# Optimization experiments

Hardware: AMD Instinct MI355X
Metric: run time of the kernel (lower is better)

## Reference

```python
import jax, jax.numpy as jnp
import numpy as np

N, E, G = 50000, 500000, 8
IN, HID, OUT, NC, H = 256, 128, 64, 10, 2
NPG = N // G  # nodes per graph
NEG_SLOPE = 0.2


def setup_inputs() -> dict:
    key = jax.random.key(0)
    ks = jax.random.split(key, 24)
    x = jax.random.normal(ks[0], (N, IN), jnp.float32)
    # edges constrained to stay within each graph, no self-loops
    src = jax.random.randint(ks[1], (E,), 0, N)
    base = (src // NPG) * NPG
    off = jax.random.randint(ks[2], (E,), 1, NPG)
    dst = base + (src - base + off) % NPG
    edge_index = jnp.stack([src, dst], axis=0).astype(jnp.int32)
    edge_attr = jax.random.uniform(ks[3], (E, 1), jnp.float32)
    batch = jnp.repeat(jnp.arange(G, dtype=jnp.int32), NPG)
    y = jax.random.randint(ks[4], (N,), 0, NC).astype(jnp.int32)

    s = 0.1
    p = {
        'W1': jax.random.normal(ks[5], (IN, H * HID), jnp.float32) * s,
        'att_src1': jax.random.normal(ks[6], (H, HID), jnp.float32) * s,
        'att_dst1': jax.random.normal(ks[7], (H, HID), jnp.float32) * s,
        'We1': jax.random.normal(ks[8], (1, H * HID), jnp.float32) * s,
        'att_edge1': jax.random.normal(ks[9], (H, HID), jnp.float32) * s,
        'b1': jnp.zeros((HID,), jnp.float32),
        'W2': jax.random.normal(ks[10], (HID, H * OUT), jnp.float32) * s,
        'att_src2': jax.random.normal(ks[11], (H, OUT), jnp.float32) * s,
        'att_dst2': jax.random.normal(ks[12], (H, OUT), jnp.float32) * s,
        'We2': jax.random.normal(ks[13], (1, H * OUT), jnp.float32) * s,
        'att_edge2': jax.random.normal(ks[14], (H, OUT), jnp.float32) * s,
        'b2': jnp.zeros((OUT,), jnp.float32),
        'Wc': jax.random.normal(ks[15], (OUT, NC), jnp.float32) * s,
        'bc': jnp.zeros((NC,), jnp.float32),
    }
    return dict(x=x, edge_index=edge_index, edge_attr=edge_attr, batch=batch, y=y, **p)


def _gat_layer(x, src, dst, eattr, W, a_src, a_dst, We, a_e, b, n_nodes, C):
    # PyG GATConv: heads=H, concat=False (mean over heads), edge_dim features.
    xp = (x @ W).reshape(n_nodes, H, C)                    # [N,H,C]
    al_s = jnp.einsum('nhc,hc->nh', xp, a_src)             # [N,H]
    al_d = jnp.einsum('nhc,hc->nh', xp, a_dst)
    ef = (eattr @ We).reshape(-1, H, C)                    # [E,H,C]
    al_e = jnp.einsum('ehc,hc->eh', ef, a_e)               # [E,H]
    alpha = jax.nn.leaky_relu(al_s[src] + al_d[dst] + al_e, NEG_SLOPE)
    # edge softmax grouped by destination (every dst has a self-loop -> no empty segs)
    m = jax.ops.segment_max(alpha, dst, num_segments=n_nodes)
    ex = jnp.exp(alpha - m[dst])
    denom = jax.ops.segment_sum(ex, dst, num_segments=n_nodes)
    w = ex / (denom[dst] + 1e-16)                          # [E,H]
    msg = xp[src] * w[:, :, None]                          # [E,H,C]
    out = jax.ops.segment_sum(msg, dst, num_segments=n_nodes)  # [N,H,C]
    return out.mean(axis=1) + b


def reference(x, edge_index, edge_attr, batch, y,
              W1, att_src1, att_dst1, We1, att_edge1, b1,
              W2, att_src2, att_dst2, We2, att_edge2, b2,
              Wc, bc):
    src, dst = edge_index[0], edge_index[1]
    # add self-loops; edge_attr fill = per-graph mean (as in the per-graph loop)
    g = batch[src]
    cnt = jax.ops.segment_sum(jnp.ones_like(edge_attr[:, 0]), g, num_segments=G)
    mean_attr = jax.ops.segment_sum(edge_attr, g, num_segments=G) / cnt[:, None]
    loop_attr = mean_attr[batch]                           # [N,1]
    ar = jnp.arange(N, dtype=src.dtype)
    src_a = jnp.concatenate([src, ar])
    dst_a = jnp.concatenate([dst, ar])
    ea = jnp.concatenate([edge_attr, loop_attr], axis=0)

    h = _gat_layer(x, src_a, dst_a, ea, W1, att_src1, att_dst1, We1, att_edge1, b1, N, HID)
    h = jax.nn.relu(h)
    h = _gat_layer(h, src_a, dst_a, ea, W2, att_src2, att_dst2, We2, att_edge2, b2, N, OUT)
    pred = h @ Wc + bc                                     # [N,NC]
    return pred, y
```

## Files before the change

### kernel.cpp

```cpp
#include <hip/hip_runtime.h>
#include <hip/hip_bf16.h>
#include <cstdint>
#include <cstddef>

#define N_NODES 50000
#define N_EDGES 500000
#define EA_EDGES 550000
#define NPG 6250
#define G_GRAPHS 8
#define IN_DIM 256
#define HID_DIM 128
#define OUT_DIM 64
#define NCLS 10
#define NEG_SLOPE 0.2f

typedef __attribute__((ext_vector_type(8))) short short8v;
typedef __attribute__((ext_vector_type(4))) float f32x4;

__device__ __forceinline__ unsigned short f2bf(float f) {
  __hip_bfloat16 h = __float2bfloat16(f);
  unsigned short u;
  __builtin_memcpy(&u, &h, 2);
  return u;
}
__device__ __forceinline__ float bf2f(unsigned short u) {
  return __uint_as_float(((unsigned)u) << 16);
}

__global__ void k_sums_degree(const int* __restrict__ src, const int* __restrict__ dst,
                              const float* __restrict__ eattr,
                              float* __restrict__ sums, float* __restrict__ cnts,
                              int* __restrict__ deg) {
  __shared__ float ls[G_GRAPHS], lc[G_GRAPHS];
  if (threadIdx.x < G_GRAPHS) { ls[threadIdx.x] = 0.f; lc[threadIdx.x] = 0.f; }
  __syncthreads();
  int stride = gridDim.x * blockDim.x;
  for (int e = blockIdx.x * blockDim.x + threadIdx.x; e < EA_EDGES; e += stride) {
    if (e < N_EDGES) {
      int g = src[e] / NPG;
      atomicAdd(&ls[g], eattr[e]);
      atomicAdd(&lc[g], 1.f);
      atomicAdd(&deg[dst[e]], 1);
    } else {
      atomicAdd(&deg[e - N_EDGES], 1);
    }
  }
  __syncthreads();
  if (threadIdx.x < G_GRAPHS) {
    atomicAdd(&sums[threadIdx.x], ls[threadIdx.x]);
    atomicAdd(&cnts[threadIdx.x], lc[threadIdx.x]);
  }
}

__global__ void k_prep(const float* __restrict__ sums, const float* __restrict__ cnts,
                       float* __restrict__ mean,
                       const float* __restrict__ We1, const float* __restrict__ ae1,
                       const float* __restrict__ We2, const float* __restrict__ ae2,
                       float* __restrict__ ce) {
  if (threadIdx.x == 0 && blockIdx.x == 0) {
    for (int g = 0; g < G_GRAPHS; ++g) mean[g] = sums[g] / cnts[g];
    for (int h = 0; h < 2; ++h) {
      float s = 0.f;
      for (int c = 0; c < HID_DIM; ++c) s += We1[h * HID_DIM + c] * ae1[h * HID_DIM + c];
      ce[h] = s;
    }
    for (int h = 0; h < 2; ++h) {
      float s = 0.f;
      for (int c = 0; c < OUT_DIM; ++c) s += We2[h * OUT_DIM + c] * ae2[h * OUT_DIM + c];
      ce[2 + h] = s;
    }
  }
}

__global__ void k_scan1(const int* __restrict__ deg, int* __restrict__ rowptr,
                        int* __restrict__ bsum, int n) {
  __shared__ int sm[1024];
  int tid = threadIdx.x;
  int i = blockIdx.x * 1024 + tid;
  int v = (i < n) ? deg[i] : 0;
  sm[tid] = v;
  __syncthreads();
  for (int off = 1; off < 1024; off <<= 1) {
    int t = (tid >= off) ? sm[tid - off] : 0;
    __syncthreads();
    if (tid >= off) sm[tid] += t;
    __syncthreads();
  }
  if (i < n) rowptr[i] = sm[tid] - v;
  if (tid == 1023) bsum[blockIdx.x] = sm[1023];
}

__global__ void k_scan2(int* __restrict__ bsum, int* __restrict__ rowptr, int nb, int n) {
  if (threadIdx.x == 0 && blockIdx.x == 0) {
    int run = 0;
    for (int i = 0; i < nb; ++i) { int v = bsum[i]; bsum[i] = run; run += v; }
    rowptr[n] = run;
  }
}

__global__ void k_scan3(int* __restrict__ rowptr, int* __restrict__ cursor,
                        const int* __restrict__ bsum, int n) {
  int i = blockIdx.x * blockDim.x + threadIdx.x;
  if (i < n) {
    int r = rowptr[i] + bsum[i >> 10];
    rowptr[i] = r;
    cursor[i] = r;
  }
}

__global__ void k_fill(const int* __restrict__ src, const int* __restrict__ dst,
                       const float* __restrict__ eattr, const float* __restrict__ mean,
                       int* __restrict__ cursor, int2* __restrict__ csr) {
  int e = blockIdx.x * blockDim.x + threadIdx.x;
  if (e >= EA_EDGES) return;
  int s, d; float a;
  if (e < N_EDGES) { s = src[e]; d = dst[e]; a = eattr[e]; }
  else { int i = e - N_EDGES; s = i; d = i; a = mean[i / NPG]; }
  int p = atomicAdd(&cursor[d], 1);
  csr[p] = make_int2(s, __float_as_int(a));
}

__global__ void k_cast_bf16(const float* __restrict__ in, unsigned short* __restrict__ out, int n8) {
  int i = blockIdx.x * blockDim.x + threadIdx.x;
  if (i >= n8) return;
  float4 a = *(const float4*)(in + (size_t)i * 8);
  float4 b = *(const float4*)(in + (size_t)i * 8 + 4);
  uint4 o;
  o.x = (unsigned)f2bf(a.x) | ((unsigned)f2bf(a.y) << 16);
  o.y = (unsigned)f2bf(a.z) | ((unsigned)f2bf(a.w) << 16);
  o.z = (unsigned)f2bf(b.x) | ((unsigned)f2bf(b.y) << 16);
  o.w = (unsigned)f2bf(b.z) | ((unsigned)f2bf(b.w) << 16);
  *(uint4*)(out + (size_t)i * 8) = o;
}

__global__ void k_cast_t(const float* __restrict__ W, unsigned short* __restrict__ Wt,
                         int K, int N) {
  int i = blockIdx.x * blockDim.x + threadIdx.x;
  if (i >= K * N) return;
  int k = i / N, n = i - k * N;
  Wt[(size_t)n * K + k] = f2bf(W[i]);
}

template <int K>
__global__ __launch_bounds__(256) void k_gemm_mfma(const unsigned short* __restrict__ A,
                                                   const unsigned short* __restrict__ Bt,
                                                   unsigned short* __restrict__ C,
                                                   int M, int Nout) {
  constexpr int BM = 128, BN = 128, BK = 64;
  __shared__ __attribute__((aligned(16))) unsigned short As[BM * BK];
  __shared__ __attribute__((aligned(16))) unsigned short Bs[BN * BK];
  const int tid = threadIdx.x;
  const int lane = tid & 63;
  const int wid = tid >> 6;
  const int wr = wid >> 1, wc = wid & 1;
  const int r0 = blockIdx.y * BM, c0 = blockIdx.x * BN;
  f32x4 acc[4][4] = {};

  for (int k0 = 0; k0 < K; k0 += BK) {
#pragma unroll
    for (int i = 0; i < 4; ++i) {
      int c = tid + i * 256;
      int row = c >> 3, kc = c & 7;
      int gr = r0 + row;
      uint4 v = make_uint4(0, 0, 0, 0);
      if (gr < M) v = *(const uint4*)(A + (size_t)gr * K + k0 + kc * 8);
      int boff = (row * 128 + kc * 16) ^ ((row & 7) << 4);
      *(uint4*)((char*)As + boff) = v;
    }
#pragma unroll
    for (int i = 0; i < 4; ++i) {
      int c = tid + i * 256;
      int row = c >> 3, kc = c & 7;
      uint4 v = *(const uint4*)(Bt + (size_t)(c0 + row) * K + k0 + kc * 8);
      int boff = (row * 128 + kc * 16) ^ ((row & 7) << 4);
      *(uint4*)((char*)Bs + boff) = v;
    }
    __syncthreads();
#pragma unroll
    for (int ks = 0; ks < 2; ++ks) {
      short8v a[4], b[4];
#pragma unroll
      for (int mi = 0; mi < 4; ++mi) {
        int row = wr * 64 + mi * 16 + (lane & 15);
        int boff = (row * 128 + ks * 64 + (lane >> 4) * 16) ^ ((row & 7) << 4);
        a[mi] = *(const short8v*)((const char*)As + boff);
      }
#pragma unroll
      for (int ni = 0; ni < 4; ++ni) {
        int row = wc * 64 + ni * 16 + (lane & 15);
        int boff = (row * 128 + ks * 64 + (lane >> 4) * 16) ^ ((row & 7) << 4);
        b[ni] = *(const short8v*)((const char*)Bs + boff);
      }
#pragma unroll
      for (int mi = 0; mi < 4; ++mi)
#pragma unroll
        for (int ni = 0; ni < 4; ++ni)
          acc[mi][ni] = __builtin_amdgcn_mfma_f32_16x16x32_bf16(a[mi], b[ni], acc[mi][ni], 0, 0, 0);
    }
    __syncthreads();
  }
#pragma unroll
  for (int mi = 0; mi < 4; ++mi) {
#pragma unroll
    for (int r = 0; r < 4; ++r) {
      int row = r0 + wr * 64 + mi * 16 + (lane >> 4) * 4 + r;
      if (row < M) {
#pragma unroll
        for (int ni = 0; ni < 4; ++ni) {
          int col = c0 + wc * 64 + ni * 16 + (lane & 15);
          C[(size_t)row * Nout + col] = f2bf(acc[mi][ni][r]);
        }
      }
    }
  }
}

template <int C>
__global__ void k_als(const unsigned short* __restrict__ xp, const float* __restrict__ a_src,
                      const float* __restrict__ a_dst, float* __restrict__ als,
                      float* __restrict__ ald) {
  constexpr int TC = 2 * C;
  constexpr int VPL = TC / 64;
  int wave = (blockIdx.x * blockDim.x + threadIdx.x) >> 6;
  int lane = threadIdx.x & 63;
  if (wave >= N_NODES) return;
  const unsigned short* row = xp + (size_t)wave * TC + lane * VPL;
  float v[VPL];
  if (VPL == 4) {
    ushort4 u = *(const ushort4*)row;
    v[0] = bf2f(u.x); v[1] = bf2f(u.y); v[2] = bf2f(u.z); v[3] = bf2f(u.w);
  } else {
    ushort2 u = *(const ushort2*)row;
    v[0] = bf2f(u.x); v[1] = bf2f(u.y);
  }
  float s_ = 0.f, d_ = 0.f;
#pragma unroll
  for (int k = 0; k < VPL; ++k) {
    s_ += v[k] * a_src[lane * VPL + k];
    d_ += v[k] * a_dst[lane * VPL + k];
  }
#pragma unroll
  for (int off = 1; off < 32; off <<= 1) {
    s_ += __shfl_xor(s_, off);
    d_ += __shfl_xor(d_, off);
  }
  if (lane == 0)  { als[2 * wave]     = s_; ald[2 * wave]     = d_; }
  if (lane == 32) { als[2 * wave + 1] = s_; ald[2 * wave + 1] = d_; }
}

template <int C, bool RELU, bool BF16OUT>
__global__ void k_aggregate(const unsigned short* __restrict__ xp,
                            const float* __restrict__ als, const float* __restrict__ ald,
                            const int* __restrict__ rowptr, const int2* __restrict__ csr,
                            const float* __restrict__ ce,
                            const float* __restrict__ bias, void* __restrict__ outv) {
  constexpr int TC = 2 * C;
  constexpr int VPL = TC / 64;
  int lane = threadIdx.x & 63;
  int wid = threadIdx.x >> 6;
  int local = (blockIdx.x >> 3) * 4 + wid;
  if (local >= NPG) return;
  int node = (blockIdx.x & 7) * NPG + local;
  int p0 = rowptr[node], p1 = rowptr[node + 1];
  int deg = p1 - p0;
  int half = lane >> 5;
  int sub = lane & 31;
  float ald_m = ald[2 * node + half];
  float ce_m = ce[half];
  float m = -1e30f, den = 0.f;
  float acc[VPL];
#pragma unroll
  for (int k = 0; k < VPL; ++k) acc[k] = 0.f;

  for (int base = 0; base < deg; base += 32) {
    int nE = min(32, deg - base);
    float a = -1e30f;
    int s = 0;
    if (sub < nE) {
      int2 md = csr[p0 + base + sub];
      s = md.x;
      float ea = __int_as_float(md.y);
      float l = als[2 * s + half] + ald_m + ce_m * ea;
      a = (l > 0.f) ? l : NEG_SLOPE * l;
    }
    float cm = a;
#pragma unroll
    for (int off = 1; off < 32; off <<= 1) cm = fmaxf(cm, __shfl_xor(cm, off));
    float nm = fmaxf(m, cm);
    float cs = __expf(m - nm);
    m = nm;
    float w = (sub < nE) ? __expf(a - m) : 0.f;
    float ws = w;
#pragma unroll
    for (int off = 1; off < 32; off <<= 1) ws += __shfl_xor(ws, off);
    den = den * cs + ws;
#pragma unroll
    for (int k = 0; k < VPL; ++k) acc[k] *= cs;
    for (int e = 0; e < nE; ++e) {
      int se = __shfl(s, e);
      float wh = __shfl(w, e | (lane & 32));
      const unsigned short* row = xp + (size_t)se * TC + lane * VPL;
      if (VPL == 4) {
        ushort4 u = *(const ushort4*)row;
        acc[0] += wh * bf2f(u.x);
        acc[1] += wh * bf2f(u.y);
        acc[2] += wh * bf2f(u.z);
        acc[3] += wh * bf2f(u.w);
      } else {
        ushort2 u = *(const ushort2*)row;
        acc[0] += wh * bf2f(u.x);
        acc[1] += wh * bf2f(u.y);
      }
    }
  }

  float deni = 1.f / (den + 1e-16f);
  float t[VPL];
#pragma unroll
  for (int k = 0; k < VPL; ++k) {
    t[k] = acc[k] * deni;
    t[k] += __shfl_xor(t[k], 32);
  }
  if (lane < 32) {
    int c = lane * VPL;
    float v[VPL];
#pragma unroll
    for (int k = 0; k < VPL; ++k) {
      v[k] = 0.5f * t[k] + bias[c + k];
      if (RELU) v[k] = fmaxf(v[k], 0.f);
    }
    if (BF16OUT) {
      unsigned short* o = (unsigned short*)outv + (size_t)node * C + c;
      if (VPL == 4) {
        ushort4 u;
        u.x = f2bf(v[0]); u.y = f2bf(v[1]); u.z = f2bf(v[2]); u.w = f2bf(v[3]);
        *(ushort4*)o = u;
      } else {
        ushort2 u; u.x = f2bf(v[0]); u.y = f2bf(v[1]);
        *(ushort2*)o = u;
      }
    } else {
      float* o = (float*)outv + (size_t)node * C + c;
#pragma unroll
      for (int k = 0; k < VPL; ++k) o[k] = v[k];
    }
  }
}

__global__ void k_classifier(const float* __restrict__ h2, const float* __restrict__ Wc,
                             const float* __restrict__ bc, const int* __restrict__ y,
                             float* __restrict__ out) {
  __shared__ float wcs[OUT_DIM * NCLS];
  __shared__ float bcs[NCLS];
  for (int i = threadIdx.x; i < OUT_DIM * NCLS; i += blockDim.x) wcs[i] = Wc[i];
  if (threadIdx.x < NCLS) bcs[threadIdx.x] = bc[threadIdx.x];
  __syncthreads();
  int n = blockIdx.x * blockDim.x + threadIdx.x;
  if (n >= N_NODES) return;
  float acc[NCLS];
#pragma unroll
  for (int j = 0; j < NCLS; ++j) acc[j] = bcs[j];
  for (int k = 0; k < OUT_DIM; ++k) {
    float v = h2[(size_t)n * OUT_DIM + k];
#pragma unroll
    for (int j = 0; j < NCLS; ++j) acc[j] += v * wcs[k * NCLS + j];
  }
#pragma unroll
  for (int j = 0; j < NCLS; ++j) out[(size_t)n * NCLS + j] = acc[j];
  out[(size_t)N_NODES * NCLS + n] = (float)y[n];
}

extern "C" void kernel_launch(void* const* d_in, const int* in_sizes, int n_in,
                              void* d_out, int out_size, void* d_ws, size_t ws_size,
                              hipStream_t stream) {
  const float* x     = (const float*)d_in[0];
  const int*   ei    = (const int*)d_in[1];
  const float* eattr = (const float*)d_in[2];
  const int*   y     = (const int*)d_in[4];
  const float* W1  = (const float*)d_in[5];
  const float* as1 = (const float*)d_in[6];
  const float* ad1 = (const float*)d_in[7];
  const float* We1 = (const float*)d_in[8];
  const float* ae1 = (const float*)d_in[9];
  const float* b1  = (const float*)d_in[10];
  const float* W2  = (const float*)d_in[11];
  const float* as2 = (const float*)d_in[12];
  const float* ad2 = (const float*)d_in[13];
  const float* We2 = (const float*)d_in[14];
  const float* ae2 = (const float*)d_in[15];
  const float* b2  = (const float*)d_in[16];
  const float* Wc  = (const float*)d_in[17];
  const float* bc  = (const float*)d_in[18];
  float* out = (float*)d_out;

  const int* src = ei;
  const int* dst = ei + N_EDGES;

  char* wsb = (char*)d_ws;
  size_t o = 0;
  auto alloc = [&](size_t bytes) { size_t r = o; o = (o + bytes + 255) & ~(size_t)255; return r; };
  size_t o_sums   = alloc(G_GRAPHS * 4);
  size_t o_cnts   = alloc(G_GRAPHS * 4);
  size_t o_mean   = alloc(G_GRAPHS * 4);
  size_t o_ce     = alloc(4 * 4);
  size_t o_bsum   = alloc(64 * 4);
  size_t o_deg    = alloc((size_t)N_NODES * 4);
  size_t o_rowptr = alloc((size_t)(N_NODES + 1) * 4);
  size_t o_cursor = alloc((size_t)N_NODES * 4);
  size_t o_csr    = alloc((size_t)EA_EDGES * 8);
  size_t o_xb     = alloc((size_t)N_NODES * IN_DIM * 2);
  size_t o_wt1    = alloc((size_t)IN_DIM * 256 * 2);
  size_t o_wt2    = alloc((size_t)HID_DIM * 128 * 2);
  size_t o_xp     = alloc((size_t)N_NODES * 256 * 2);
  size_t o_h1b    = alloc((size_t)N_NODES * HID_DIM * 2);
  size_t o_h2     = alloc((size_t)N_NODES * OUT_DIM * 4);
  size_t o_als    = alloc((size_t)N_NODES * 2 * 4);
  size_t o_ald    = alloc((size_t)N_NODES * 2 * 4);
  (void)ws_size;

  float* sums   = (float*)(wsb + o_sums);
  float* cnts   = (float*)(wsb + o_cnts);
  float* mean   = (float*)(wsb + o_mean);
  float* ce     = (float*)(wsb + o_ce);
  int*   bsum   = (int*)(wsb + o_bsum);
  int*   deg    = (int*)(wsb + o_deg);
  int*   rowptr = (int*)(wsb + o_rowptr);
  int*   cursor = (int*)(wsb + o_cursor);
  int2*  csr    = (int2*)(wsb + o_csr);
  unsigned short* xb  = (unsigned short*)(wsb + o_xb);
  unsigned short* wt1 = (unsigned short*)(wsb + o_wt1);
  unsigned short* wt2 = (unsigned short*)(wsb + o_wt2);
  unsigned short* xp  = (unsigned short*)(wsb + o_xp);
  unsigned short* h1b = (unsigned short*)(wsb + o_h1b);
  float* h2     = (float*)(wsb + o_h2);
  float* als    = (float*)(wsb + o_als);
  float* ald    = (float*)(wsb + o_ald);

  hipMemsetAsync(sums, 0, G_GRAPHS * 4 * 2, stream);
  hipMemsetAsync(deg, 0, (size_t)N_NODES * 4, stream);

  k_cast_bf16<<<(N_NODES * IN_DIM / 8 + 255) / 256, 256, 0, stream>>>(x, xb, N_NODES * IN_DIM / 8);
  k_cast_t<<<(IN_DIM * 256 + 255) / 256, 256, 0, stream>>>(W1, wt1, IN_DIM, 256);
  k_cast_t<<<(HID_DIM * 128 + 255) / 256, 256, 0, stream>>>(W2, wt2, HID_DIM, 128);

  k_sums_degree<<<512, 256, 0, stream>>>(src, dst, eattr, sums, cnts, deg);
  k_prep<<<1, 64, 0, stream>>>(sums, cnts, mean, We1, ae1, We2, ae2, ce);

  int eaBlocks = (EA_EDGES + 255) / 256;
  int nScanBlocks = (N_NODES + 1023) / 1024;
  k_scan1<<<nScanBlocks, 1024, 0, stream>>>(deg, rowptr, bsum, N_NODES);
  k_scan2<<<1, 64, 0, stream>>>(bsum, rowptr, nScanBlocks, N_NODES);
  k_scan3<<<(N_NODES + 255) / 256, 256, 0, stream>>>(rowptr, cursor, bsum, N_NODES);
  k_fill<<<eaBlocks, 256, 0, stream>>>(src, dst, eattr, mean, cursor, csr);

  int aggBlocks = G_GRAPHS * ((NPG + 3) / 4);

  {
    dim3 grid(256 / 128, (N_NODES + 127) / 128);
    k_gemm_mfma<IN_DIM><<<grid, 256, 0, stream>>>(xb, wt1, xp, N_NODES, 256);
  }
  k_als<HID_DIM><<<(N_NODES + 3) / 4, 256, 0, stream>>>(xp, as1, ad1, als, ald);
  k_aggregate<HID_DIM, true, true><<<aggBlocks, 256, 0, stream>>>(
      xp, als, ald, rowptr, csr, ce, b1, h1b);

  {
    dim3 grid(128 / 128, (N_NODES + 127) / 128);
    k_gemm_mfma<HID_DIM><<<grid, 256, 0, stream>>>(h1b, wt2, xp, N_NODES, 128);
  }
  k_als<OUT_DIM><<<(N_NODES + 3) / 4, 256, 0, stream>>>(xp, as2, ad2, als, ald);
  k_aggregate<OUT_DIM, false, false><<<aggBlocks, 256, 0, stream>>>(
      xp, als, ald, rowptr, csr, ce + 2, b2, h2);

  k_classifier<<<(N_NODES + 255) / 256, 256, 0, stream>>>(h2, Wc, bc, y, out);
}
```

Before: 340.9 us.

## Fuse attention logits into GEMM epilogue and batch neighbor gathers in aggregation

Removes the separate k_als kernels. The GEMM epilogue now computes per-row source and destination attention dot products from the accumulators. It reduces them across 16 lanes and atomically adds them into als/ald, which are zeroed with a memset beforehand. The aggregation inner loop is also unrolled to issue 8 neighbor-row gathers before accumulating, to expose more memory-level parallelism. The costs are float atomics, which make the summation order nondeterministic, two extra memsets, and padded gathers of row 0 with zero weight.

```diff
diff --git a/kernel.cpp b/kernel.cpp
--- a/kernel.cpp
+++ b/kernel.cpp
@@ -145,7 +145,11 @@
 __global__ __launch_bounds__(256) void k_gemm_mfma(const unsigned short* __restrict__ A,
                                                    const unsigned short* __restrict__ Bt,
                                                    unsigned short* __restrict__ C,
-                                                   int M, int Nout) {
+                                                   int M, int Nout,
+                                                   const float* __restrict__ a_src,
+                                                   const float* __restrict__ a_dst,
+                                                   float* __restrict__ als,
+                                                   float* __restrict__ ald) {
   constexpr int BM = 128, BN = 128, BK = 64;
   __shared__ __attribute__((aligned(16))) unsigned short As[BM * BK];
   __shared__ __attribute__((aligned(16))) unsigned short Bs[BN * BK];
@@ -199,6 +203,7 @@
     }
     __syncthreads();
   }
+
 #pragma unroll
   for (int mi = 0; mi < 4; ++mi) {
 #pragma unroll
@@ -213,39 +218,39 @@
       }
     }
   }
-}
-
-template <int C>
-__global__ void k_als(const unsigned short* __restrict__ xp, const float* __restrict__ a_src,
-                      const float* __restrict__ a_dst, float* __restrict__ als,
-                      float* __restrict__ ald) {
-  constexpr int TC = 2 * C;
-  constexpr int VPL = TC / 64;
-  int wave = (blockIdx.x * blockDim.x + threadIdx.x) >> 6;
-  int lane = threadIdx.x & 63;
-  if (wave >= N_NODES) return;
-  const unsigned short* row = xp + (size_t)wave * TC + lane * VPL;
-  float v[VPL];
-  if (VPL == 4) {
-    ushort4 u = *(const ushort4*)row;
-    v[0] = bf2f(u.x); v[1] = bf2f(u.y); v[2] = bf2f(u.z); v[3] = bf2f(u.w);
-  } else {
-    ushort2 u = *(const ushort2*)row;
-    v[0] = bf2f(u.x); v[1] = bf2f(u.y);
-  }
-  float s_ = 0.f, d_ = 0.f;
-#pragma unroll
-  for (int k = 0; k < VPL; ++k) {
-    s_ += v[k] * a_src[lane * VPL + k];
-    d_ += v[k] * a_dst[lane * VPL + k];
-  }
-#pragma unroll
-  for (int off = 1; off < 32; off <<= 1) {
-    s_ += __shfl_xor(s_, off);
-    d_ += __shfl_xor(d_, off);
-  }
-  if (lane == 0)  { als[2 * wave]     = s_; ald[2 * wave]     = d_; }
-  if (lane == 32) { als[2 * wave + 1] = s_; ald[2 * wave + 1] = d_; }
+
+  {
+    int headc = (c0 + wc * 64) / (Nout >> 1);
+    float asv[4], adv[4];
+#pragma unroll
+    for (int ni = 0; ni < 4; ++ni) {
+      int col = c0 + wc * 64 + ni * 16 + (lane & 15);
+      asv[ni] = a_src[col];
+      adv[ni] = a_dst[col];
+    }
+#pragma unroll
+    for (int mi = 0; mi < 4; ++mi) {
+#pragma unroll
+      for (int r = 0; r < 4; ++r) {
+        float ps = 0.f, pd = 0.f;
+#pragma unroll
+        for (int ni = 0; ni < 4; ++ni) {
+          ps += acc[mi][ni][r] * asv[ni];
+          pd += acc[mi][ni][r] * adv[ni];
+        }
+#pragma unroll
+        for (int off = 1; off < 16; off <<= 1) {
+          ps += __shfl_xor(ps, off);
+          pd += __shfl_xor(pd, off);
+        }
+        int row = r0 + wr * 64 + mi * 16 + (lane >> 4) * 4 + r;
+        if ((lane & 15) == 0 && row < M) {
+          atomicAdd(&als[2 * row + headc], ps);
+          atomicAdd(&ald[2 * row + headc], pd);
+        }
+      }
+    }
+  }
 }
 
 template <int C, bool RELU, bool BF16OUT>
@@ -276,6 +281,7 @@
     int nE = min(32, deg - base);
     float a = -1e30f;
     int s = 0;
+    float w = 0.f;
     if (sub < nE) {
       int2 md = csr[p0 + base + sub];
       s = md.x;
@@ -289,27 +295,43 @@
     float nm = fmaxf(m, cm);
     float cs = __expf(m - nm);
     m = nm;
-    float w = (sub < nE) ? __expf(a - m) : 0.f;
+    if (sub < nE) w = __expf(a - m);
     float ws = w;
 #pragma unroll
     for (int off = 1; off < 32; off <<= 1) ws += __shfl_xor(ws, off);
     den = den * cs + ws;
 #pragma unroll
     for (int k = 0; k < VPL; ++k) acc[k] *= cs;
-    for (int e = 0; e < nE; ++e) {
-      int se = __shfl(s, e);
-      float wh = __shfl(w, e | (lane & 32));
-      const unsigned short* row = xp + (size_t)se * TC + lane * VPL;
+    for (int e0 = 0; e0 < nE; e0 += 8) {
+      int se[8]; float wh[8];
+#pragma unroll
+      for (int j = 0; j < 8; ++j) {
+        int e = e0 + j;
+        se[j] = __shfl(s, e);
+        wh[j] = __shfl(w, e | (lane & 32));
+      }
       if (VPL == 4) {
-        ushort4 u = *(const ushort4*)row;
-        acc[0] += wh * bf2f(u.x);
-        acc[1] += wh * bf2f(u.y);
-        acc[2] += wh * bf2f(u.z);
-        acc[3] += wh * bf2f(u.w);
+        ushort4 u[8];
+#pragma unroll
+        for (int j = 0; j < 8; ++j)
+          u[j] = *(const ushort4*)(xp + (size_t)se[j] * TC + lane * VPL);
+#pragma unroll
+        for (int j = 0; j < 8; ++j) {
+          acc[0] += wh[j] * bf2f(u[j].x);
+          acc[1] += wh[j] * bf2f(u[j].y);
+          acc[2] += wh[j] * bf2f(u[j].z);
+          acc[3] += wh[j] * bf2f(u[j].w);
+        }
       } else {
-        ushort2 u = *(const ushort2*)row;
-        acc[0] += wh * bf2f(u.x);
-        acc[1] += wh * bf2f(u.y);
+        ushort2 u[8];
+#pragma unroll
+        for (int j = 0; j < 8; ++j)
+          u[j] = *(const ushort2*)(xp + (size_t)se[j] * TC + lane * VPL);
+#pragma unroll
+        for (int j = 0; j < 8; ++j) {
+          acc[0] += wh[j] * bf2f(u[j].x);
+          acc[1] += wh[j] * bf2f(u[j].y);
+        }
       }
     }
   }
@@ -435,6 +457,7 @@
   float* h2     = (float*)(wsb + o_h2);
   float* als    = (float*)(wsb + o_als);
   float* ald    = (float*)(wsb + o_ald);
+  size_t alsald_bytes = (o_ald - o_als) + (size_t)N_NODES * 2 * 4;
 
   hipMemsetAsync(sums, 0, G_GRAPHS * 4 * 2, stream);
   hipMemsetAsync(deg, 0, (size_t)N_NODES * 4, stream);
@@ -455,19 +478,21 @@
 
   int aggBlocks = G_GRAPHS * ((NPG + 3) / 4);
 
+  hipMemsetAsync(als, 0, alsald_bytes, stream);
   {
     dim3 grid(256 / 128, (N_NODES + 127) / 128);
-    k_gemm_mfma<IN_DIM><<<grid, 256, 0, stream>>>(xb, wt1, xp, N_NODES, 256);
-  }
-  k_als<HID_DIM><<<(N_NODES + 3) / 4, 256, 0, stream>>>(xp, as1, ad1, als, ald);
+    k_gemm_mfma<IN_DIM><<<grid, 256, 0, stream>>>(xb, wt1, xp, N_NODES, 256,
+                                                  as1, ad1, als, ald);
+  }
   k_aggregate<HID_DIM, true, true><<<aggBlocks, 256, 0, stream>>>(
       xp, als, ald, rowptr, csr, ce, b1, h1b);
 
+  hipMemsetAsync(als, 0, alsald_bytes, stream);
   {
     dim3 grid(128 / 128, (N_NODES + 127) / 128);
-    k_gemm_mfma<HID_DIM><<<grid, 256, 0, stream>>>(h1b, wt2, xp, N_NODES, 128);
-  }
-  k_als<OUT_DIM><<<(N_NODES + 3) / 4, 256, 0, stream>>>(xp, as2, ad2, als, ald);
+    k_gemm_mfma<HID_DIM><<<grid, 256, 0, stream>>>(h1b, wt2, xp, N_NODES, 128,
+                                                   as2, ad2, als, ald);
+  }
   k_aggregate<OUT_DIM, false, false><<<aggBlocks, 256, 0, stream>>>(
       xp, als, ald, rowptr, csr, ce + 2, b2, h2);
 
```

Measured after the change: 333.2 us. -2.3%, faster.
